# Kernel optimization log

Measured on AMD Instinct MI355X. Metric: run time of the kernel, lower is better.

## Reference

```python
import jax, jax.numpy as jnp
import numpy as np

# ---- static irreps config: 128x0e + 128x1e + 128x2e (in == out) ----
MULS = (128, 128, 128)
LS = (0, 1, 2)
DIM = sum(m * (2 * l + 1) for m, l in zip(MULS, LS))  # 1152
N_EDGES = 32768


def _m_indices(m):
    # column indices selected by m_in_mask[m] / m_out_mask[m], in ascending order
    idx, off = [], 0
    for mul, l in zip(MULS, LS):
        k = 2 * l + 1
        if l >= m:
            for j in range(mul):
                base = off + j * k
                if m == 0:
                    idx.append(base + l)
                else:
                    idx.extend([base + l - m, base + l + m])
        off += mul * k
    return np.asarray(idx, dtype=np.int32)

IDX = [_m_indices(m) for m in range(3)]

_S3 = float(np.sqrt(3.0) / 2.0)
J_MATS = {
    1: np.array([[0.0, 1, 0], [1, 0, 0], [0, 0, -1]], np.float32),
    2: np.array([[0.0, 0, 0, -1, 0],
                 [0, 1, 0, 0, 0],
                 [0, 0, -0.5, 0, -_S3],
                 [-1, 0, 0, 0, 0],
                 [0, 0, -_S3, 0, 0.5]], np.float32),
}


def _z_rot(a, l):
    # matches torch _z_rot: diag cos(f*a) + anti-diag (flipped) sin(f*a), f = l..-l
    freqs = jnp.arange(l, -l - 1, -1, dtype=a.dtype)
    d = jnp.cos(freqs * a[:, None])   # (n, 2l+1)
    ad = jnp.sin(freqs * a[:, None])
    eye = jnp.eye(2 * l + 1, dtype=a.dtype)
    return d[..., None] * eye + jnp.flip(ad[..., None] * eye, axis=-1)


def _wigner(l, alpha, beta):
    Jl = jnp.asarray(J_MATS[l], dtype=alpha.dtype)
    return _z_rot(alpha, l) @ Jl @ _z_rot(beta, l) @ Jl  # gamma = 0 -> Z(0)=I


def setup_inputs() -> dict:
    key = jax.random.key(0)
    ks = jax.random.split(key, 6)
    x = jax.random.normal(ks[0], (N_EDGES, DIM), jnp.float32)
    R = jax.random.normal(ks[1], (N_EDGES, 3), jnp.float32)
    W0 = jax.random.normal(ks[2], (384, 384), jnp.float32) / np.sqrt(384.0)
    b0 = 0.01 * jax.random.normal(ks[3], (384,), jnp.float32)
    W1 = jax.random.normal(ks[4], (512, 256), jnp.float32) / np.sqrt(2.0 * 256.0)
    W2 = jax.random.normal(ks[5], (256, 128), jnp.float32) / np.sqrt(2.0 * 128.0)
    return {"x": x, "R": R, "W0": W0, "b0": b0, "W1": W1, "W2": W2}


def _forward(x, R, W0, b0, W1, W2):
    n = x.shape[0]
    # xyz_to_angles(R[:, [1, 2, 0]])
    v = jnp.take(R, jnp.array([1, 2, 0]), axis=1)
    v = v / jnp.clip(jnp.linalg.norm(v, axis=1, keepdims=True), 1e-12)
    beta = jnp.arccos(jnp.clip(v[:, 1], -1.0, 1.0))
    alpha = jnp.arctan2(v[:, 0], v[:, 2])
    D1 = _wigner(1, alpha, beta)  # (n,3,3)
    D2 = _wigner(2, alpha, beta)  # (n,5,5)

    # rotate input irreps (l > 0) into edge-aligned frame: D^T x per l-block
    b1 = x[:, 128:512].reshape(n, 128, 3)
    b2 = x[:, 512:1152].reshape(n, 128, 5)
    r1 = jnp.einsum('nji,nmj->nmi', D1, b1).reshape(n, -1)
    r2 = jnp.einsum('nji,nmj->nmi', D2, b2).reshape(n, -1)
    x_rot = jnp.concatenate([x[:, :128], r1, r2], axis=1)

    out = jnp.zeros((n, DIM), dtype=x.dtype)

    # m = 0 path: gather m=0 components, zero out l=0 scalar inputs, fc0
    seg0 = x_rot[:, IDX[0]]  # (n, 384)
    seg0 = jnp.concatenate([jnp.zeros_like(seg0[:, :128]), seg0[:, 128:]], axis=1)
    out = out.at[:, IDX[0]].add(seg0 @ W0.T + b0)

    # m >= 1 paths: gather, complex-style small GEMM, scatter back
    for m, W in ((1, W1), (2, W2)):
        seg = x_rot[:, IDX[m]].reshape(n, 2, -1)          # (n, 2, num_in_m)
        y = jnp.einsum('ncj,kj->nck', seg, W)              # (n, 2, 2*num_out_m)
        no = y.shape[-1] // 2
        out_re = y[:, 0, :no] - y[:, 1, no:]
        out_im = y[:, 0, no:] + y[:, 1, :no]
        out = out.at[:, IDX[m]].add(jnp.concatenate([out_re, out_im], axis=1))

    # rotate output irreps (l > 0) back to the original frame: D y per l-block
    o1 = jnp.einsum('nij,nmj->nmi', D1, out[:, 128:512].reshape(n, 128, 3)).reshape(n, -1)
    o2 = jnp.einsum('nij,nmj->nmi', D2, out[:, 512:1152].reshape(n, 128, 5)).reshape(n, -1)
    return jnp.concatenate([out[:, :128], o1, o2], axis=1)


def reference(x, R, W0, b0, W1, W2):
    return _forward(x, R, W0, b0, W1, W2)
```

## Files before the change

kernel.cpp:

```cpp
#include <hip/hip_runtime.h>
#include <cstddef>
#include <cstdint>


typedef _Float16 f16x8 __attribute__((ext_vector_type(8)));
typedef _Float16 f16x2 __attribute__((ext_vector_type(2)));
typedef float    f32x4 __attribute__((ext_vector_type(4)));

#define AS1 __attribute__((address_space(1)))
#define AS3 __attribute__((address_space(3)))

__device__ __forceinline__ void mm3(const float* A, const float* B, float* C) {
#pragma unroll
  for (int i = 0; i < 3; ++i)
#pragma unroll
    for (int j = 0; j < 3; ++j)
      C[i*3+j] = fmaf(A[i*3+0], B[0*3+j], fmaf(A[i*3+1], B[1*3+j], A[i*3+2]*B[2*3+j]));
}

__device__ __forceinline__ void mm5(const float* A, const float* B, float* C) {
#pragma unroll
  for (int i = 0; i < 5; ++i)
#pragma unroll
    for (int j = 0; j < 5; ++j) {
      float s = 0.f;
#pragma unroll
      for (int k = 0; k < 5; ++k) s = fmaf(A[i*5+k], B[k*5+j], s);
      C[i*5+j] = s;
    }
}

__global__ __launch_bounds__(256) void wigner_k(const float* __restrict__ R,
                                                float* __restrict__ D1buf,
                                                float* __restrict__ D2buf, int n) {
  int e = blockIdx.x*256 + threadIdx.x;
  if (e >= n) return;
  float r0 = R[3*e+0], r1 = R[3*e+1], r2 = R[3*e+2];
  float v0 = r1, v1 = r2, v2 = r0;
  float nrm = fmaxf(sqrtf(v0*v0 + v1*v1 + v2*v2), 1e-12f);
  float inv = 1.0f/nrm;
  v0 *= inv; v1 *= inv; v2 *= inv;

  float cb = fminf(fmaxf(v1, -1.f), 1.f);
  float sb = sqrtf(fmaxf(1.f - cb*cb, 0.f));
  float h = sqrtf(v0*v0 + v2*v2);
  float ca, sa;
  if (h > 1e-20f) { float ih = 1.f/h; ca = v2*ih; sa = v0*ih; }
  else            { ca = 1.f; sa = 0.f; }

  {
    float Za[9] = {ca,0,sa, 0,1,0, -sa,0,ca};
    float Zb[9] = {cb,0,sb, 0,1,0, -sb,0,cb};
    const float J1[9] = {0,1,0, 1,0,0, 0,0,-1};
    float T[9], T2[9], D1[9];
    mm3(Zb, J1, T); mm3(J1, T, T2); mm3(Za, T2, D1);
#pragma unroll
    for (int i = 0; i < 9; ++i) D1buf[(size_t)e*9 + i] = D1[i];
  }
  {
    float c2a = ca*ca - sa*sa, s2a = 2.f*ca*sa;
    float c2b = cb*cb - sb*sb, s2b = 2.f*cb*sb;
    float Za2[25] = {
      c2a, 0,   0, 0,   s2a,
      0,   ca,  0, sa,  0,
      0,   0,   1, 0,   0,
      0,  -sa,  0, ca,  0,
     -s2a, 0,   0, 0,   c2a};
    float Zb2[25] = {
      c2b, 0,   0, 0,   s2b,
      0,   cb,  0, sb,  0,
      0,   0,   1, 0,   0,
      0,  -sb,  0, cb,  0,
     -s2b, 0,   0, 0,   c2b};
    const float S3 = 0.8660254037844386f;
    const float J2[25] = {
      0, 0, 0,    -1, 0,
      0, 1, 0,     0, 0,
      0, 0, -0.5f, 0, -S3,
     -1, 0, 0,     0, 0,
      0, 0, -S3,   0, 0.5f};
    float T[25], T2[25], D2[25];
    mm5(Zb2, J2, T); mm5(J2, T, T2); mm5(Za2, T2, D2);
#pragma unroll
    for (int i = 0; i < 25; ++i) D2buf[(size_t)e*25 + i] = D2[i];
  }
}

__global__ __launch_bounds__(256) void build_mats(const float* __restrict__ W0,
                                                  const float* __restrict__ b0,
                                                  const float* __restrict__ W1,
                                                  const float* __restrict__ W2,
                                                  _Float16* __restrict__ M0,
                                                  float* __restrict__ B0,
                                                  _Float16* __restrict__ M1,
                                                  _Float16* __restrict__ M2) {
  int i = blockIdx.x*256 + threadIdx.x;
  if (i < 98304) {
    int k = i >> 8, j = i & 255;
    M0[i] = (_Float16)W0[k*384 + 128 + j];
  } else if (i < 98688) {
    B0[i - 98304] = b0[i - 98304];
  } else if (i < 360832) {
    int idx = i - 98688;
    int k = idx >> 9, j = idx & 511;
    float val;
    if (k < 256) val = (j < 256) ? W1[k*256 + j] : -W1[(k+256)*256 + (j-256)];
    else         val = (j < 256) ? W1[k*256 + j] :  W1[(k-256)*256 + (j-256)];
    M1[idx] = (_Float16)val;
  } else if (i < 426368) {
    int idx = i - 360832;
    int k = idx >> 8, j = idx & 255;
    float val;
    if (k < 128) val = (j < 128) ? W2[k*128 + j] : -W2[(k+128)*128 + (j-128)];
    else         val = (j < 128) ? W2[k*128 + j] :  W2[(k-128)*128 + (j-128)];
    M2[idx] = (_Float16)val;
  }
}

__global__ __launch_bounds__(256) void rotate_gather(const float* __restrict__ x,
                                                     const float* __restrict__ D1buf,
                                                     const float* __restrict__ D2buf,
                                                     _Float16* __restrict__ U, int n) {
  __shared__ float xs[4][1152];
  __shared__ __align__(16) _Float16 us16[4][1024];
  const int w = threadIdx.x >> 6;
  const int lane = threadIdx.x & 63;
  const int e = blockIdx.x*4 + w;

  const float4* xr = (const float4*)(x + (size_t)e*1152);
  float4* xsw = (float4*)xs[w];
#pragma unroll
  for (int i = 0; i < 4; ++i) xsw[lane + i*64] = xr[lane + i*64];
  if (lane < 32) xsw[lane + 256] = xr[lane + 256];

  float d1[9], d2[25];
#pragma unroll
  for (int i = 0; i < 9; ++i) d1[i] = D1buf[(size_t)e*9 + i];
#pragma unroll
  for (int i = 0; i < 25; ++i) d2[i] = D2buf[(size_t)e*25 + i];

  __syncthreads();

#pragma unroll
  for (int hh = 0; hh < 2; ++hh) {
    int c = lane + 64*hh;
    float b0 = xs[w][128 + 3*c + 0];
    float b1 = xs[w][128 + 3*c + 1];
    float b2 = xs[w][128 + 3*c + 2];
    float r0 = fmaf(d1[0], b0, fmaf(d1[3], b1, d1[6]*b2));
    float r1 = fmaf(d1[1], b0, fmaf(d1[4], b1, d1[7]*b2));
    float r2 = fmaf(d1[2], b0, fmaf(d1[5], b1, d1[8]*b2));
    us16[w][c] = (_Float16)r1;
    { f16x2 t; t[0] = (_Float16)r0; t[1] = (_Float16)r2;
      *(f16x2*)&us16[w][256 + 2*c] = t; }

    float q0 = xs[w][512 + 5*c + 0];
    float q1 = xs[w][512 + 5*c + 1];
    float q2 = xs[w][512 + 5*c + 2];
    float q3 = xs[w][512 + 5*c + 3];
    float q4 = xs[w][512 + 5*c + 4];
    float rr[5];
#pragma unroll
    for (int i = 0; i < 5; ++i)
      rr[i] = fmaf(d2[0*5+i], q0, fmaf(d2[1*5+i], q1, fmaf(d2[2*5+i], q2,
               fmaf(d2[3*5+i], q3, d2[4*5+i]*q4))));
    us16[w][128 + c] = (_Float16)rr[2];
    { f16x2 t; t[0] = (_Float16)rr[1]; t[1] = (_Float16)rr[3];
      *(f16x2*)&us16[w][512 + 2*c] = t; }
    { f16x2 t; t[0] = (_Float16)rr[0]; t[1] = (_Float16)rr[4];
      if (c < 64) *(f16x2*)&us16[w][768 + 2*c] = t;
      else        *(f16x2*)&us16[w][896 + 2*(c-64)] = t; }
  }
  __syncthreads();

  f16x8* Ur = (f16x8*)(U + (size_t)e*1024);
  const f16x8* usw = (const f16x8*)us16[w];
#pragma unroll
  for (int i = 0; i < 2; ++i) Ur[i*64 + lane] = usw[i*64 + lane];
}

__global__ __launch_bounds__(256) void gemm_mfma(const _Float16* __restrict__ U,
                                                 const _Float16* __restrict__ M0,
                                                 const float* __restrict__ B0,
                                                 const _Float16* __restrict__ M1,
                                                 const _Float16* __restrict__ M2,
                                                 float* __restrict__ C, int n) {
  const int y = blockIdx.y;
  int K, Aoff, Coff, colTile;
  const _Float16* Mp;
  const float* bias = nullptr;
  if (y < 3)      { K = 256; Aoff = 0;   Coff = 0;   colTile = y;     Mp = M0; bias = B0; }
  else if (y < 7) { K = 512; Aoff = 256; Coff = 384; colTile = y - 3; Mp = M1; }
  else            { K = 256; Aoff = 768; Coff = 896; colTile = y - 7; Mp = M2; }
  const int colBase = colTile * 128;
  const int rowBase = blockIdx.x * 128;

  __shared__ __align__(16) _Float16 Als[128*64];
  __shared__ __align__(16) _Float16 Bls[128*64];

  const int t  = threadIdx.x;
  const int w  = t >> 6, l = t & 63;
  const int wr = w >> 1, wc = w & 1;
  const int fr = l & 15, g0 = l >> 4;

  const char* Ag = (const char*)(U + (size_t)rowBase*1024 + Aoff);
  const char* Bg = (const char*)(Mp + (size_t)colBase*K);
  const int sprime = (l & 7) ^ (l >> 3);
  const int rl = l >> 3;

  f32x4 acc[4][4];
#pragma unroll
  for (int m = 0; m < 4; ++m)
#pragma unroll
    for (int nn = 0; nn < 4; ++nn) { f32x4 z = {0.f,0.f,0.f,0.f}; acc[m][nn] = z; }

  for (int kk = 0; kk < K; kk += 64) {
#pragma unroll
    for (int cc = 0; cc < 4; ++cc) {
      const int c = w + cc*4;
      const int r = c*8 + rl;
      __builtin_amdgcn_global_load_lds(
          (const AS1 void*)(Ag + (size_t)r*2048 + (size_t)kk*2 + sprime*16),
          (AS3 void*)((char*)Als + c*1024), 16, 0, 0);
      __builtin_amdgcn_global_load_lds(
          (const AS1 void*)(Bg + (size_t)r*(size_t)(K*2) + (size_t)kk*2 + sprime*16),
          (AS3 void*)((char*)Bls + c*1024), 16, 0, 0);
    }
    __syncthreads();

#pragma unroll
    for (int h = 0; h < 2; ++h) {
      const int sidx = h*4 + g0;
      f16x8 af[4], bf[4];
#pragma unroll
      for (int m = 0; m < 4; ++m) {
        const int row = wr*64 + m*16 + fr;
        af[m] = *(const f16x8*)((const char*)Als + row*128 + ((sidx ^ (row & 7))*16));
      }
#pragma unroll
      for (int nn = 0; nn < 4; ++nn) {
        const int col = wc*64 + nn*16 + fr;
        bf[nn] = *(const f16x8*)((const char*)Bls + col*128 + ((sidx ^ (col & 7))*16));
      }
#pragma unroll
      for (int m = 0; m < 4; ++m)
#pragma unroll
        for (int nn = 0; nn < 4; ++nn)
          acc[m][nn] = __builtin_amdgcn_mfma_f32_16x16x32_f16(af[m], bf[nn], acc[m][nn], 0, 0, 0);
    }
    __syncthreads();
  }

  float bv[4];
#pragma unroll
  for (int nn = 0; nn < 4; ++nn)
    bv[nn] = bias ? bias[colBase + wc*64 + nn*16 + fr] : 0.f;
#pragma unroll
  for (int m = 0; m < 4; ++m) {
    const int row0 = rowBase + wr*64 + m*16 + g0*4;
#pragma unroll
    for (int nn = 0; nn < 4; ++nn) {
      const int vc = Coff + colBase + wc*64 + nn*16 + fr;
#pragma unroll
      for (int j = 0; j < 4; ++j)
        C[(size_t)(row0 + j)*1152 + vc] = acc[m][nn][j] + bv[nn];
    }
  }
}

__global__ __launch_bounds__(256) void rotate_back(float* __restrict__ out,
                                                   const float* __restrict__ D1buf,
                                                   const float* __restrict__ D2buf, int n) {
  __shared__ float vs[4][1152];
  __shared__ float fs[4][1152];
  const int w = threadIdx.x >> 6;
  const int lane = threadIdx.x & 63;
  const int e = blockIdx.x*4 + w;

  const float4* vr = (const float4*)(out + (size_t)e*1152);
  float4* vsw = (float4*)vs[w];
#pragma unroll
  for (int i = 0; i < 4; ++i) vsw[lane + i*64] = vr[lane + i*64];
  if (lane < 32) vsw[lane + 256] = vr[lane + 256];

  float d1[9], d2[25];
#pragma unroll
  for (int i = 0; i < 9; ++i) d1[i] = D1buf[(size_t)e*9 + i];
#pragma unroll
  for (int i = 0; i < 25; ++i) d2[i] = D2buf[(size_t)e*25 + i];

  __syncthreads();

  fs[w][lane]      = vs[w][lane];
  fs[w][64 + lane] = vs[w][64 + lane];

#pragma unroll
  for (int hh = 0; hh < 2; ++hh) {
    int c = lane + 64*hh;
    float p0 = vs[w][384 + 2*c];
    float p1 = vs[w][128 + c];
    float p2 = vs[w][384 + 2*c + 1];
    fs[w][128 + 3*c + 0] = fmaf(d1[0], p0, fmaf(d1[1], p1, d1[2]*p2));
    fs[w][128 + 3*c + 1] = fmaf(d1[3], p0, fmaf(d1[4], p1, d1[5]*p2));
    fs[w][128 + 3*c + 2] = fmaf(d1[6], p0, fmaf(d1[7], p1, d1[8]*p2));

    float q0, q4;
    if (c < 64) { q0 = vs[w][896 + 2*c];        q4 = vs[w][896 + 2*c + 1]; }
    else        { q0 = vs[w][1024 + 2*(c-64)];  q4 = vs[w][1024 + 2*(c-64) + 1]; }
    float q1 = vs[w][640 + 2*c];
    float q2 = vs[w][256 + c];
    float q3 = vs[w][640 + 2*c + 1];
#pragma unroll
    for (int i = 0; i < 5; ++i)
      fs[w][512 + 5*c + i] = fmaf(d2[i*5+0], q0, fmaf(d2[i*5+1], q1, fmaf(d2[i*5+2], q2,
                              fmaf(d2[i*5+3], q3, d2[i*5+4]*q4))));
  }
  __syncthreads();

  float4* orow = (float4*)(out + (size_t)e*1152);
  const float4* fsw = (const float4*)fs[w];
#pragma unroll
  for (int i = 0; i < 4; ++i) orow[lane + i*64] = fsw[lane + i*64];
  if (lane < 32) orow[lane + 256] = fsw[lane + 256];
}

extern "C" void kernel_launch(void* const* d_in, const int* in_sizes, int n_in,
                              void* d_out, int out_size, void* d_ws, size_t ws_size,
                              hipStream_t stream) {
  const float* x  = (const float*)d_in[0];
  const float* R  = (const float*)d_in[1];
  const float* W0 = (const float*)d_in[2];
  const float* b0 = (const float*)d_in[3];
  const float* W1 = (const float*)d_in[4];
  const float* W2 = (const float*)d_in[5];
  float* out = (float*)d_out;

  const int n = in_sizes[0] / 1152;

  char* wsb = (char*)d_ws;
  _Float16* U16  = (_Float16*)wsb;
  float* D1buf   = (float*)(wsb + (size_t)n*1024*2);
  float* D2buf   = D1buf + (size_t)n*9;
  _Float16* M0h  = (_Float16*)(D2buf + (size_t)n*25);
  _Float16* M1h  = M0h + 98304;
  _Float16* M2h  = M1h + 262144;
  float* B0f     = (float*)(M2h + 65536);

  wigner_k<<<(n + 255)/256, 256, 0, stream>>>(R, D1buf, D2buf, n);
  build_mats<<<(426368 + 255)/256, 256, 0, stream>>>(W0, b0, W1, W2, M0h, B0f, M1h, M2h);
  rotate_gather<<<n/4, 256, 0, stream>>>(x, D1buf, D2buf, U16, n);
  dim3 ggrid(n/128, 9);
  gemm_mfma<<<ggrid, 256, 0, stream>>>(U16, M0h, B0f, M1h, M2h, out, n);
  rotate_back<<<n/4, 256, 0, stream>>>(out, D1buf, D2buf, n);
}
```

Before: 383.7 us.

## Drop LDS staging in rotate kernels, swizzle GEMM grid, add out-of-place rotate-back

rotate_gather now uses one thread per (edge, channel) and reads x and writes U straight from global memory, with no shared-memory staging or barriers. The GEMM grid becomes 1D and is remapped so groups of 8 row tiles share the same weight section, which should improve L2 reuse of the weight tiles. When the workspace is large enough, the GEMM writes to a separate fp32 buffer and a new rotate_back2 kernel reads from it and writes the final output directly, again without LDS. The catch is that global accesses become strided and less coalesced (3- and 5-element strides), and the extra buffer means additional DRAM traffic.

```diff
diff --git a/kernel.cpp b/kernel.cpp
--- a/kernel.cpp
+++ b/kernel.cpp
@@ -121,17 +121,10 @@
                                                      const float* __restrict__ D1buf,
                                                      const float* __restrict__ D2buf,
                                                      _Float16* __restrict__ U, int n) {
-  __shared__ float xs[4][1152];
-  __shared__ __align__(16) _Float16 us16[4][1024];
-  const int w = threadIdx.x >> 6;
-  const int lane = threadIdx.x & 63;
-  const int e = blockIdx.x*4 + w;
-
-  const float4* xr = (const float4*)(x + (size_t)e*1152);
-  float4* xsw = (float4*)xs[w];
-#pragma unroll
-  for (int i = 0; i < 4; ++i) xsw[lane + i*64] = xr[lane + i*64];
-  if (lane < 32) xsw[lane + 256] = xr[lane + 256];
+  const int tid = blockIdx.x*256 + threadIdx.x;
+  const int e = tid >> 7;
+  const int c = tid & 127;
+  if (e >= n) return;
 
   float d1[9], d2[25];
 #pragma unroll
@@ -139,44 +132,35 @@
 #pragma unroll
   for (int i = 0; i < 25; ++i) d2[i] = D2buf[(size_t)e*25 + i];
 
-  __syncthreads();
-
-#pragma unroll
-  for (int hh = 0; hh < 2; ++hh) {
-    int c = lane + 64*hh;
-    float b0 = xs[w][128 + 3*c + 0];
-    float b1 = xs[w][128 + 3*c + 1];
-    float b2 = xs[w][128 + 3*c + 2];
-    float r0 = fmaf(d1[0], b0, fmaf(d1[3], b1, d1[6]*b2));
-    float r1 = fmaf(d1[1], b0, fmaf(d1[4], b1, d1[7]*b2));
-    float r2 = fmaf(d1[2], b0, fmaf(d1[5], b1, d1[8]*b2));
-    us16[w][c] = (_Float16)r1;
-    { f16x2 t; t[0] = (_Float16)r0; t[1] = (_Float16)r2;
-      *(f16x2*)&us16[w][256 + 2*c] = t; }
-
-    float q0 = xs[w][512 + 5*c + 0];
-    float q1 = xs[w][512 + 5*c + 1];
-    float q2 = xs[w][512 + 5*c + 2];
-    float q3 = xs[w][512 + 5*c + 3];
-    float q4 = xs[w][512 + 5*c + 4];
-    float rr[5];
-#pragma unroll
-    for (int i = 0; i < 5; ++i)
-      rr[i] = fmaf(d2[0*5+i], q0, fmaf(d2[1*5+i], q1, fmaf(d2[2*5+i], q2,
-               fmaf(d2[3*5+i], q3, d2[4*5+i]*q4))));
-    us16[w][128 + c] = (_Float16)rr[2];
-    { f16x2 t; t[0] = (_Float16)rr[1]; t[1] = (_Float16)rr[3];
-      *(f16x2*)&us16[w][512 + 2*c] = t; }
-    { f16x2 t; t[0] = (_Float16)rr[0]; t[1] = (_Float16)rr[4];
-      if (c < 64) *(f16x2*)&us16[w][768 + 2*c] = t;
-      else        *(f16x2*)&us16[w][896 + 2*(c-64)] = t; }
-  }
-  __syncthreads();
-
-  f16x8* Ur = (f16x8*)(U + (size_t)e*1024);
-  const f16x8* usw = (const f16x8*)us16[w];
-#pragma unroll
-  for (int i = 0; i < 2; ++i) Ur[i*64 + lane] = usw[i*64 + lane];
+  const float* xr = x + (size_t)e*1152;
+  _Float16* Ur = U + (size_t)e*1024;
+
+  float b0 = xr[128 + 3*c + 0];
+  float b1 = xr[128 + 3*c + 1];
+  float b2 = xr[128 + 3*c + 2];
+  float r0 = fmaf(d1[0], b0, fmaf(d1[3], b1, d1[6]*b2));
+  float r1 = fmaf(d1[1], b0, fmaf(d1[4], b1, d1[7]*b2));
+  float r2 = fmaf(d1[2], b0, fmaf(d1[5], b1, d1[8]*b2));
+  Ur[c] = (_Float16)r1;
+  { f16x2 t; t[0] = (_Float16)r0; t[1] = (_Float16)r2;
+    *(f16x2*)&Ur[256 + 2*c] = t; }
+
+  float q0 = xr[512 + 5*c + 0];
+  float q1 = xr[512 + 5*c + 1];
+  float q2 = xr[512 + 5*c + 2];
+  float q3 = xr[512 + 5*c + 3];
+  float q4 = xr[512 + 5*c + 4];
+  float rr[5];
+#pragma unroll
+  for (int i = 0; i < 5; ++i)
+    rr[i] = fmaf(d2[0*5+i], q0, fmaf(d2[1*5+i], q1, fmaf(d2[2*5+i], q2,
+             fmaf(d2[3*5+i], q3, d2[4*5+i]*q4))));
+  Ur[128 + c] = (_Float16)rr[2];
+  { f16x2 t; t[0] = (_Float16)rr[1]; t[1] = (_Float16)rr[3];
+    *(f16x2*)&Ur[512 + 2*c] = t; }
+  { f16x2 t; t[0] = (_Float16)rr[0]; t[1] = (_Float16)rr[4];
+    if (c < 64) *(f16x2*)&Ur[768 + 2*c] = t;
+    else        *(f16x2*)&Ur[896 + 2*(c-64)] = t; }
 }
 
 __global__ __launch_bounds__(256) void gemm_mfma(const _Float16* __restrict__ U,
@@ -185,15 +169,20 @@
                                                  const _Float16* __restrict__ M1,
                                                  const _Float16* __restrict__ M2,
                                                  float* __restrict__ C, int n) {
-  const int y = blockIdx.y;
+  const int bid = blockIdx.x;
+  const int x8 = bid & 7;
+  const int g  = bid >> 3;
+  const int rr = g / 9;
+  const int sec = g - rr*9;
+  const int rowBase = (rr*8 + x8) * 128;
+
   int K, Aoff, Coff, colTile;
   const _Float16* Mp;
   const float* bias = nullptr;
-  if (y < 3)      { K = 256; Aoff = 0;   Coff = 0;   colTile = y;     Mp = M0; bias = B0; }
-  else if (y < 7) { K = 512; Aoff = 256; Coff = 384; colTile = y - 3; Mp = M1; }
-  else            { K = 256; Aoff = 768; Coff = 896; colTile = y - 7; Mp = M2; }
+  if (sec < 3)      { K = 256; Aoff = 0;   Coff = 0;   colTile = sec;     Mp = M0; bias = B0; }
+  else if (sec < 7) { K = 512; Aoff = 256; Coff = 384; colTile = sec - 3; Mp = M1; }
+  else              { K = 256; Aoff = 768; Coff = 896; colTile = sec - 7; Mp = M2; }
   const int colBase = colTile * 128;
-  const int rowBase = blockIdx.x * 128;
 
   __shared__ __align__(16) _Float16 Als[128*64];
   __shared__ __align__(16) _Float16 Bls[128*64];
@@ -268,9 +257,48 @@
   }
 }
 
-__global__ __launch_bounds__(256) void rotate_back(float* __restrict__ out,
-                                                   const float* __restrict__ D1buf,
-                                                   const float* __restrict__ D2buf, int n) {
+__global__ __launch_bounds__(256) void rotate_back2(const float* __restrict__ V,
+                                                    float* __restrict__ out,
+                                                    const float* __restrict__ D1buf,
+                                                    const float* __restrict__ D2buf, int n) {
+  const int tid = blockIdx.x*256 + threadIdx.x;
+  const int e = tid >> 7;
+  const int c = tid & 127;
+  if (e >= n) return;
+
+  float d1[9], d2[25];
+#pragma unroll
+  for (int i = 0; i < 9; ++i) d1[i] = D1buf[(size_t)e*9 + i];
+#pragma unroll
+  for (int i = 0; i < 25; ++i) d2[i] = D2buf[(size_t)e*25 + i];
+
+  const float* Vr = V + (size_t)e*1152;
+  float* orow = out + (size_t)e*1152;
+
+  orow[c] = Vr[c];
+
+  float2 pp = *(const float2*)&Vr[384 + 2*c];
+  float p0 = pp.x, p2 = pp.y;
+  float p1 = Vr[128 + c];
+  orow[128 + 3*c + 0] = fmaf(d1[0], p0, fmaf(d1[1], p1, d1[2]*p2));
+  orow[128 + 3*c + 1] = fmaf(d1[3], p0, fmaf(d1[4], p1, d1[5]*p2));
+  orow[128 + 3*c + 2] = fmaf(d1[6], p0, fmaf(d1[7], p1, d1[8]*p2));
+
+  float2 qq = (c < 64) ? *(const float2*)&Vr[896 + 2*c]
+                       : *(const float2*)&Vr[1024 + 2*(c-64)];
+  float q0 = qq.x, q4 = qq.y;
+  float2 q13 = *(const float2*)&Vr[640 + 2*c];
+  float q1 = q13.x, q3 = q13.y;
+  float q2 = Vr[256 + c];
+#pragma unroll
+  for (int i = 0; i < 5; ++i)
+    orow[512 + 5*c + i] = fmaf(d2[i*5+0], q0, fmaf(d2[i*5+1], q1, fmaf(d2[i*5+2], q2,
+                           fmaf(d2[i*5+3], q3, d2[i*5+4]*q4))));
+}
+
+__global__ __launch_bounds__(256) void rotate_back_ip(float* __restrict__ out,
+                                                      const float* __restrict__ D1buf,
+                                                      const float* __restrict__ D2buf, int n) {
   __shared__ float vs[4][1152];
   __shared__ float fs[4][1152];
   const int w = threadIdx.x >> 6;
@@ -337,19 +365,31 @@
 
   const int n = in_sizes[0] / 1152;
 
-  char* wsb = (char*)d_ws;
-  _Float16* U16  = (_Float16*)wsb;
-  float* D1buf   = (float*)(wsb + (size_t)n*1024*2);
-  float* D2buf   = D1buf + (size_t)n*9;
-  _Float16* M0h  = (_Float16*)(D2buf + (size_t)n*25);
-  _Float16* M1h  = M0h + 98304;
-  _Float16* M2h  = M1h + 262144;
-  float* B0f     = (float*)(M2h + 65536);
+  const size_t szV  = (size_t)n*1152*4;
+  const size_t szU  = (size_t)n*1024*2;
+  const size_t szD1 = (size_t)n*9*4;
+  const size_t szD2 = (size_t)n*25*4;
+  const size_t szM  = 196608 + 524288 + 131072 + 1536;
+  const bool vInWs = ws_size >= szV + szU + szD1 + szD2 + szM;
+
+  char* p = (char*)d_ws;
+  float* V32 = nullptr;
+  if (vInWs) { V32 = (float*)p; p += szV; }
+  _Float16* U16 = (_Float16*)p;            p += szU;
+  float* D1buf  = (float*)p;               p += szD1;
+  float* D2buf  = (float*)p;               p += szD2;
+  _Float16* M0h = (_Float16*)p;            p += 196608;
+  _Float16* M1h = (_Float16*)p;            p += 524288;
+  _Float16* M2h = (_Float16*)p;            p += 131072;
+  float* B0f    = (float*)p;
 
   wigner_k<<<(n + 255)/256, 256, 0, stream>>>(R, D1buf, D2buf, n);
   build_mats<<<(426368 + 255)/256, 256, 0, stream>>>(W0, b0, W1, W2, M0h, B0f, M1h, M2h);
-  rotate_gather<<<n/4, 256, 0, stream>>>(x, D1buf, D2buf, U16, n);
-  dim3 ggrid(n/128, 9);
-  gemm_mfma<<<ggrid, 256, 0, stream>>>(U16, M0h, B0f, M1h, M2h, out, n);
-  rotate_back<<<n/4, 256, 0, stream>>>(out, D1buf, D2buf, n);
-}
+  rotate_gather<<<n/2, 256, 0, stream>>>(x, D1buf, D2buf, U16, n);
+
+  float* V = vInWs ? V32 : out;
+  gemm_mfma<<<(n/128)*9, 256, 0, stream>>>(U16, M0h, B0f, M1h, M2h, V, n);
+
+  if (vInWs) rotate_back2<<<n/2, 256, 0, stream>>>(V32, out, D1buf, D2buf, n);
+  else       rotate_back_ip<<<n/4, 256, 0, stream>>>(out, D1buf, D2buf, n);
+}
```

Result: faster. 367.8 us (-4.1%).
